# Performance work log

Measured on AMD Instinct MI355X. Metric: run time of the kernel, lower is better.

## Reference

```python
import jax, jax.numpy as jnp
import numpy as np

B, S, D, H = 2, 2048, 1024, 16

def setup_inputs() -> dict:
    key = jax.random.key(0)
    ks = jax.random.split(key, 5)
    s = 0.02
    return {
        "x": jax.random.normal(ks[0], (B, S, D), dtype=jnp.float32),
        "Wq": jax.random.normal(ks[1], (D, D), dtype=jnp.float32) * s,
        "bq": jnp.zeros((D,), dtype=jnp.float32),
        "Wk": jax.random.normal(ks[2], (D, D), dtype=jnp.float32) * s,
        "bk": jnp.zeros((D,), dtype=jnp.float32),
        "Wv": jax.random.normal(ks[3], (D, D), dtype=jnp.float32) * s,
        "bv": jnp.zeros((D,), dtype=jnp.float32),
        "Wp": jax.random.normal(ks[4], (D, D), dtype=jnp.float32) * s,
        "bp": jnp.zeros((D,), dtype=jnp.float32),
    }

def reference(x, Wq, bq, Wk, bk, Wv, bv, Wp, bp):
    b, s, d = x.shape
    hd = d // H
    # QKV projections, split into heads: [b, H, s, hd]
    q = (x @ Wq.T + bq).reshape(b, s, H, hd).transpose(0, 2, 1, 3)
    k = (x @ Wk.T + bk).reshape(b, s, H, hd).transpose(0, 2, 1, 3)
    v = (x @ Wv.T + bv).reshape(b, s, H, hd).transpose(0, 2, 1, 3)
    # NOTE: original scales by 1/sqrt(embedding_size), not head_dim
    att = jnp.einsum("bhqd,bhkd->bhqk", q, k) / jnp.sqrt(jnp.float32(d))
    causal = jnp.tril(jnp.ones((s, s), dtype=bool))
    att = jnp.where(causal[None, None], att, -jnp.inf)
    att = jax.nn.softmax(att, axis=-1)
    y = jnp.einsum("bhqk,bhkd->bhqd", att, v)
    y = y.transpose(0, 2, 1, 3).reshape(b, s, d)
    return y @ Wp.T + bp
```

## Files before the change

### kernel.cpp

```cpp
#include <hip/hip_runtime.h>
#include <hip/hip_bf16.h>

#define B_  2
#define S_  2048
#define D_  1024
#define H_  16
#define HD_ 64

typedef float  f32x4 __attribute__((ext_vector_type(4)));
typedef __bf16 bf16x8 __attribute__((ext_vector_type(8)));

__device__ __forceinline__ unsigned short f2bf(float f) {
    __bf16 h = (__bf16)f;
    return __builtin_bit_cast(unsigned short, h);
}

__device__ __forceinline__ void gload_lds16(const unsigned short* g, unsigned short* l) {
    __builtin_amdgcn_global_load_lds(
        (const __attribute__((address_space(1))) unsigned int*)g,
        (__attribute__((address_space(3))) unsigned int*)l, 16, 0, 0);
}

__global__ __launch_bounds__(256) void cvt5(
    const float* __restrict__ x,  const float* __restrict__ wq,
    const float* __restrict__ wk, const float* __restrict__ wv,
    const float* __restrict__ wp,
    unsigned short* __restrict__ xb, unsigned short* __restrict__ wqkv,
    unsigned short* __restrict__ wpb)
{
    const int bid = blockIdx.x;
    const float* src; unsigned short* dst; int off;
    if (bid < 4096)      { src = x;  dst = xb;              off = bid * 1024; }
    else if (bid < 5120) { src = wq; dst = wqkv;            off = (bid - 4096) * 1024; }
    else if (bid < 6144) { src = wk; dst = wqkv + (1<<20);  off = (bid - 5120) * 1024; }
    else if (bid < 7168) { src = wv; dst = wqkv + (2<<20);  off = (bid - 6144) * 1024; }
    else                 { src = wp; dst = wpb;             off = (bid - 7168) * 1024; }
    const int i = off + threadIdx.x * 4;
    float4 v = *reinterpret_cast<const float4*>(src + i);
    ushort4 o;
    o.x = f2bf(v.x); o.y = f2bf(v.y); o.z = f2bf(v.z); o.w = f2bf(v.w);
    *reinterpret_cast<ushort4*>(dst + i) = o;
}

__global__ __launch_bounds__(256, 3) void gemm128_qkv(
    const unsigned short* __restrict__ A,
    const unsigned short* __restrict__ Bm,
    const float* __restrict__ bias,
    void* __restrict__ C0, void* __restrict__ C1, void* __restrict__ C2,
    int M, int N, int K)
{
    __shared__ unsigned short As[128 * 64];
    __shared__ unsigned short Bs[128 * 64];
    const int tid  = threadIdx.x;
    const int lane = tid & 63;
    const int w    = tid >> 6;
    const int wm   = w >> 1, wn = w & 1;
    const int m0   = blockIdx.x << 7, n0 = blockIdx.y << 7;
    const int l15  = lane & 15, l4 = lane >> 4;
    const int r8   = lane >> 3;
    const int c8   = (lane & 7) << 3;

    f32x4 acc[4][4] = {};

    for (int k0 = 0; k0 < K; k0 += 64) {
        if (k0) __syncthreads();
        #pragma unroll
        for (int i = 0; i < 4; ++i) {
            const int row = i * 32 + w * 8;
            gload_lds16(A  + (size_t)(m0 + row + r8) * K + k0 + c8, As + row * 64);
            gload_lds16(Bm + (size_t)(n0 + row + r8) * K + k0 + c8, Bs + row * 64);
        }
        __syncthreads();
        #pragma unroll
        for (int kk = 0; kk < 2; ++kk) {
            bf16x8 af[4], bf[4];
            #pragma unroll
            for (int mi = 0; mi < 4; ++mi)
                af[mi] = *reinterpret_cast<const bf16x8*>(&As[(wm * 64 + mi * 16 + l15) * 64 + kk * 32 + l4 * 8]);
            #pragma unroll
            for (int ni = 0; ni < 4; ++ni)
                bf[ni] = *reinterpret_cast<const bf16x8*>(&Bs[(wn * 64 + ni * 16 + l15) * 64 + kk * 32 + l4 * 8]);
            #pragma unroll
            for (int mi = 0; mi < 4; ++mi)
                #pragma unroll
                for (int ni = 0; ni < 4; ++ni)
                    acc[mi][ni] = __builtin_amdgcn_mfma_f32_16x16x32_bf16(af[mi], bf[ni], acc[mi][ni], 0, 0, 0);
        }
    }

    const int region = n0 >> 10;
    #pragma unroll
    for (int mi = 0; mi < 4; ++mi) {
        #pragma unroll
        for (int ni = 0; ni < 4; ++ni) {
            const int colg = n0 + wn * 64 + ni * 16 + l15;
            const float bv = bias[colg];
            const int rowb = m0 + wm * 64 + mi * 16 + l4 * 4;
            const int cl = colg & 1023;
            if (region < 2) {
                unsigned short* C = (unsigned short*)(region ? C1 : C0);
                #pragma unroll
                for (int j = 0; j < 4; ++j)
                    C[(size_t)(rowb + j) * 1024 + cl] = f2bf(acc[mi][ni][j] + bv);
            } else {
                ushort4 pk;
                pk.x = f2bf(acc[mi][ni][0] + bv);
                pk.y = f2bf(acc[mi][ni][1] + bv);
                pk.z = f2bf(acc[mi][ni][2] + bv);
                pk.w = f2bf(acc[mi][ni][3] + bv);
                const int bb = rowb >> 11, s = rowb & (S_ - 1);
                unsigned short* vt = (unsigned short*)C2 +
                    ((size_t)(bb * H_ + (cl >> 6)) * HD_ + (cl & 63)) * S_ + s;
                *reinterpret_cast<ushort4*>(vt) = pk;
            }
        }
    }
}

__global__ __launch_bounds__(256, 2) void gemm64_proj(
    const unsigned short* __restrict__ A,
    const unsigned short* __restrict__ Bm,
    const float* __restrict__ bias,
    float* __restrict__ C,
    int M, int N, int K)
{
    __shared__ unsigned short As[64 * 64];
    __shared__ unsigned short Bs[128 * 64];
    const int tid  = threadIdx.x;
    const int lane = tid & 63;
    const int w    = tid >> 6;
    const int m0   = blockIdx.x << 6, n0 = blockIdx.y << 7;
    const int l15  = lane & 15, l4 = lane >> 4;
    const int r8   = lane >> 3;
    const int c8   = (lane & 7) << 3;

    f32x4 acc[4][2] = {};

    for (int k0 = 0; k0 < K; k0 += 64) {
        if (k0) __syncthreads();
        #pragma unroll
        for (int i = 0; i < 6; ++i) {
            const int c = w * 6 + i;
            if (c < 8)
                gload_lds16(A  + (size_t)(m0 + c * 8 + r8) * K + k0 + c8, As + c * 512);
            else
                gload_lds16(Bm + (size_t)(n0 + (c - 8) * 8 + r8) * K + k0 + c8, Bs + (c - 8) * 512);
        }
        __syncthreads();
        #pragma unroll
        for (int kk = 0; kk < 2; ++kk) {
            bf16x8 af[4], bf[2];
            #pragma unroll
            for (int mi = 0; mi < 4; ++mi)
                af[mi] = *reinterpret_cast<const bf16x8*>(&As[(mi * 16 + l15) * 64 + kk * 32 + l4 * 8]);
            #pragma unroll
            for (int ni = 0; ni < 2; ++ni)
                bf[ni] = *reinterpret_cast<const bf16x8*>(&Bs[(w * 32 + ni * 16 + l15) * 64 + kk * 32 + l4 * 8]);
            #pragma unroll
            for (int mi = 0; mi < 4; ++mi)
                #pragma unroll
                for (int ni = 0; ni < 2; ++ni)
                    acc[mi][ni] = __builtin_amdgcn_mfma_f32_16x16x32_bf16(af[mi], bf[ni], acc[mi][ni], 0, 0, 0);
        }
    }

    #pragma unroll
    for (int mi = 0; mi < 4; ++mi) {
        #pragma unroll
        for (int ni = 0; ni < 2; ++ni) {
            const int colg = n0 + w * 32 + ni * 16 + l15;
            const float bv = bias[colg];
            const int rowb = m0 + mi * 16 + l4 * 4;
            #pragma unroll
            for (int j = 0; j < 4; ++j)
                C[(size_t)(rowb + j) * N + colg] = acc[mi][ni][j] + bv;
        }
    }
}

#define SC_ 0.04508422f
__global__ __launch_bounds__(64, 2) void attn7(
    const unsigned short* __restrict__ qb,
    const unsigned short* __restrict__ kb,
    const unsigned short* __restrict__ vt,
    unsigned short* __restrict__ yb)
{
    __shared__ unsigned short Plds[32][88];

    const int lane = threadIdx.x;
    const int l15  = lane & 15, l4 = lane >> 4;

    const int bid  = blockIdx.x;
    const int xcd  = bid & 7;
    const int idx  = bid >> 3;
    const int hb   = xcd * 4 + (idx >> 6);
    const int j32  = idx & 31;
    const int qi   = ((idx >> 5) & 1) ? j32 : 63 - j32;
    const int h    = hb & 15, b = hb >> 4;

    const int q0w  = qi * 32;
    const size_t baseTok = (size_t)b * S_;
    const unsigned short* kgh = kb + baseTok * D_ + h * HD_;
    const unsigned short* vth = vt + (size_t)(b * H_ + h) * HD_ * S_;

    bf16x8 qf[2][2];
    #pragma unroll
    for (int m = 0; m < 2; ++m)
        #pragma unroll
        for (int kh = 0; kh < 2; ++kh)
            qf[m][kh] = *reinterpret_cast<const bf16x8*>(
                qb + (baseTok + q0w + m * 16 + l15) * D_ + h * HD_ + kh * 32 + l4 * 8);

    f32x4 o_acc[2][4] = {};
    float l_part[2][4] = {};

    const int nkv = (q0w + 95) >> 6;

    bf16x8 kf[4][2];
    #pragma unroll
    for (int kvb = 0; kvb < 4; ++kvb)
        #pragma unroll
        for (int kh = 0; kh < 2; ++kh)
            kf[kvb][kh] = *reinterpret_cast<const bf16x8*>(
                kgh + (size_t)(kvb * 16 + l15) * D_ + kh * 32 + l4 * 8);

    for (int t = 0; t < nkv; ++t) {
        const int kv0 = t << 6;
        const bool last = (t == nkv - 1);

        f32x4 s0[4] = {}, s1[4] = {};
        __builtin_amdgcn_s_setprio(1);
        #pragma unroll
        for (int kvb = 0; kvb < 4; ++kvb)
            #pragma unroll
            for (int kh = 0; kh < 2; ++kh)
                s0[kvb] = __builtin_amdgcn_mfma_f32_16x16x32_bf16(
                    qf[0][kh], kf[kvb][kh], s0[kvb], 0, 0, 0);
        #pragma unroll
        for (int kvb = 0; kvb < 4; ++kvb)
            #pragma unroll
            for (int kh = 0; kh < 2; ++kh)
                s1[kvb] = __builtin_amdgcn_mfma_f32_16x16x32_bf16(
                    qf[1][kh], kf[kvb][kh], s1[kvb], 0, 0, 0);
        __builtin_amdgcn_s_setprio(0);

        if (t + 1 < nkv) {
            #pragma unroll
            for (int kvb = 0; kvb < 4; ++kvb)
                #pragma unroll
                for (int kh = 0; kh < 2; ++kh)
                    kf[kvb][kh] = *reinterpret_cast<const bf16x8*>(
                        kgh + (size_t)(kv0 + 64 + kvb * 16 + l15) * D_ + kh * 32 + l4 * 8);
        }

        bf16x8 vf0[4];
        #pragma unroll
        for (int nb = 0; nb < 4; ++nb)
            vf0[nb] = *reinterpret_cast<const bf16x8*>(
                vth + (size_t)(nb * 16 + l15) * S_ + kv0 + l4 * 8);

        const int r = l4 * 4;
        if (!last) {
            #pragma unroll
            for (int j = 0; j < 4; ++j) {
                float p0 = exp2f(s0[0][j] * SC_), p1 = exp2f(s0[1][j] * SC_);
                float p2 = exp2f(s0[2][j] * SC_), p3 = exp2f(s0[3][j] * SC_);
                l_part[0][j] += (p0 + p1) + (p2 + p3);
                Plds[r + j][l15]      = f2bf(p0);
                Plds[r + j][16 + l15] = f2bf(p1);
                Plds[r + j][32 + l15] = f2bf(p2);
                Plds[r + j][48 + l15] = f2bf(p3);
            }
            #pragma unroll
            for (int j = 0; j < 4; ++j) {
                float p0 = exp2f(s1[0][j] * SC_), p1 = exp2f(s1[1][j] * SC_);
                float p2 = exp2f(s1[2][j] * SC_), p3 = exp2f(s1[3][j] * SC_);
                l_part[1][j] += (p0 + p1) + (p2 + p3);
                Plds[16 + r + j][l15]      = f2bf(p0);
                Plds[16 + r + j][16 + l15] = f2bf(p1);
                Plds[16 + r + j][32 + l15] = f2bf(p2);
                Plds[16 + r + j][48 + l15] = f2bf(p3);
            }
        } else {
            #pragma unroll
            for (int j = 0; j < 4; ++j) {
                const int rowg = q0w + r + j;
                float p[4];
                #pragma unroll
                for (int kvb = 0; kvb < 4; ++kvb) {
                    const bool ok = (kv0 + kvb * 16 + l15 <= rowg);
                    p[kvb] = ok ? exp2f(s0[kvb][j] * SC_) : 0.f;
                    Plds[r + j][kvb * 16 + l15] = f2bf(p[kvb]);
                }
                l_part[0][j] += (p[0] + p[1]) + (p[2] + p[3]);
            }
            #pragma unroll
            for (int j = 0; j < 4; ++j) {
                const int rowg = q0w + 16 + r + j;
                float p[4];
                #pragma unroll
                for (int kvb = 0; kvb < 4; ++kvb) {
                    const bool ok = (kv0 + kvb * 16 + l15 <= rowg);
                    p[kvb] = ok ? exp2f(s1[kvb][j] * SC_) : 0.f;
                    Plds[16 + r + j][kvb * 16 + l15] = f2bf(p[kvb]);
                }
                l_part[1][j] += (p[0] + p[1]) + (p[2] + p[3]);
            }
        }

        bf16x8 vf1[4];
        #pragma unroll
        for (int nb = 0; nb < 4; ++nb)
            vf1[nb] = *reinterpret_cast<const bf16x8*>(
                vth + (size_t)(nb * 16 + l15) * S_ + kv0 + 32 + l4 * 8);

        {
            bf16x8 pf0 = *reinterpret_cast<const bf16x8*>(&Plds[l15][l4 * 8]);
            bf16x8 pf1 = *reinterpret_cast<const bf16x8*>(&Plds[16 + l15][l4 * 8]);
            __builtin_amdgcn_s_setprio(1);
            #pragma unroll
            for (int nb = 0; nb < 4; ++nb) {
                o_acc[0][nb] = __builtin_amdgcn_mfma_f32_16x16x32_bf16(pf0, vf0[nb], o_acc[0][nb], 0, 0, 0);
                o_acc[1][nb] = __builtin_amdgcn_mfma_f32_16x16x32_bf16(pf1, vf0[nb], o_acc[1][nb], 0, 0, 0);
            }
            __builtin_amdgcn_s_setprio(0);
        }
        {
            bf16x8 pf0 = *reinterpret_cast<const bf16x8*>(&Plds[l15][32 + l4 * 8]);
            bf16x8 pf1 = *reinterpret_cast<const bf16x8*>(&Plds[16 + l15][32 + l4 * 8]);
            __builtin_amdgcn_s_setprio(1);
            #pragma unroll
            for (int nb = 0; nb < 4; ++nb) {
                o_acc[0][nb] = __builtin_amdgcn_mfma_f32_16x16x32_bf16(pf0, vf1[nb], o_acc[0][nb], 0, 0, 0);
                o_acc[1][nb] = __builtin_amdgcn_mfma_f32_16x16x32_bf16(pf1, vf1[nb], o_acc[1][nb], 0, 0, 0);
            }
            __builtin_amdgcn_s_setprio(0);
        }
    }

    float l[8];
    #pragma unroll
    for (int m = 0; m < 2; ++m)
        #pragma unroll
        for (int j = 0; j < 4; ++j)
            l[m * 4 + j] = l_part[m][j];
    #pragma unroll
    for (int st = 1; st <= 8; st <<= 1) {
        float tv[8];
        #pragma unroll
        for (int i = 0; i < 8; ++i) tv[i] = __shfl_xor(l[i], st);
        #pragma unroll
        for (int i = 0; i < 8; ++i) l[i] += tv[i];
    }
    #pragma unroll
    for (int m = 0; m < 2; ++m) {
        #pragma unroll
        for (int j = 0; j < 4; ++j) {
            const float inv = 1.0f / l[m * 4 + j];
            const int rowg = q0w + m * 16 + l4 * 4 + j;
            unsigned short* yp = yb + (baseTok + rowg) * D_ + h * HD_ + l15;
            #pragma unroll
            for (int nb = 0; nb < 4; ++nb)
                yp[nb * 16] = f2bf(o_acc[m][nb][j] * inv);
        }
    }
}

extern "C" void kernel_launch(void* const* d_in, const int* in_sizes, int n_in,
                              void* d_out, int out_size, void* d_ws, size_t ws_size,
                              hipStream_t stream)
{
    const float* x  = (const float*)d_in[0];
    const float* Wq = (const float*)d_in[1];
    const float* bq = (const float*)d_in[2];
    const float* Wk = (const float*)d_in[3];
    const float* bk = (const float*)d_in[4];
    const float* Wv = (const float*)d_in[5];
    const float* bv = (const float*)d_in[6];
    const float* Wp = (const float*)d_in[7];
    const float* bp = (const float*)d_in[8];

    char* ws = (char*)d_ws;
    const size_t MB = 1024 * 1024;
    unsigned short* xb    = (unsigned short*)(ws);
    unsigned short* wqkvb = (unsigned short*)(ws + 8 * MB);
    unsigned short* wpb   = (unsigned short*)(ws + 14 * MB);
    unsigned short* qbuf  = (unsigned short*)(ws + 16 * MB);
    unsigned short* kbuf  = (unsigned short*)(ws + 24 * MB);
    unsigned short* vtbf  = (unsigned short*)(ws + 32 * MB);
    unsigned short* ybuf  = (unsigned short*)(ws + 40 * MB);
    float*          bcat  = (float*)(ws + 48 * MB);

    const int M = B_ * S_;

    cvt5<<<8192, 256, 0, stream>>>(x, Wq, Wk, Wv, Wp, xb, wqkvb, wpb);
    hipMemcpyAsync(bcat,          bq, D_ * sizeof(float), hipMemcpyDeviceToDevice, stream);
    hipMemcpyAsync(bcat + D_,     bk, D_ * sizeof(float), hipMemcpyDeviceToDevice, stream);
    hipMemcpyAsync(bcat + 2 * D_, bv, D_ * sizeof(float), hipMemcpyDeviceToDevice, stream);

    gemm128_qkv<<<dim3(M / 128, 3072 / 128, 1), 256, 0, stream>>>(
        xb, wqkvb, bcat, qbuf, kbuf, vtbf, M, 3072, D_);

    attn7<<<2048, 64, 0, stream>>>(qbuf, kbuf, vtbf, ybuf);

    gemm64_proj<<<dim3(M / 64, D_ / 128, 1), 256, 0, stream>>>(
        ybuf, wpb, bp, (float*)d_out, M, D_, D_);
}
```

Baseline: 219.3 us.

## Split attention KV range across two blocks and add combine kernel

The attention kernel now splits each query tile's causal KV range into two halves handled by separate blocks. Each block writes unnormalized partial outputs (bf16) and row sums to workspace, and a new combine kernel adds them and normalizes. The goal is more parallelism and better balance for the long causal rows, with occupancy hint raised to 4. The bias copies are also folded into the conversion kernel to remove three memcpy launches. In exchange it adds an extra launch, extra global traffic, and rounding of the partial outputs to bf16 before they are summed.

```diff
diff --git a/kernel.cpp b/kernel.cpp
--- a/kernel.cpp
+++ b/kernel.cpp
@@ -14,6 +14,9 @@
     __bf16 h = (__bf16)f;
     return __builtin_bit_cast(unsigned short, h);
 }
+__device__ __forceinline__ float bf2f(unsigned short u) {
+    return (float)__builtin_bit_cast(__bf16, u);
+}
 
 __device__ __forceinline__ void gload_lds16(const unsigned short* g, unsigned short* l) {
     __builtin_amdgcn_global_load_lds(
@@ -24,11 +27,19 @@
 __global__ __launch_bounds__(256) void cvt5(
     const float* __restrict__ x,  const float* __restrict__ wq,
     const float* __restrict__ wk, const float* __restrict__ wv,
-    const float* __restrict__ wp,
+    const float* __restrict__ wp, const float* __restrict__ bq,
+    const float* __restrict__ bk, const float* __restrict__ bv,
     unsigned short* __restrict__ xb, unsigned short* __restrict__ wqkv,
-    unsigned short* __restrict__ wpb)
+    unsigned short* __restrict__ wpb, float* __restrict__ bcat)
 {
     const int bid = blockIdx.x;
+    if (bid >= 8192) {
+        const float* s = (bid == 8192) ? bq : (bid == 8193) ? bk : bv;
+        const int i = threadIdx.x * 4;
+        *reinterpret_cast<float4*>(bcat + (bid - 8192) * 1024 + i) =
+            *reinterpret_cast<const float4*>(s + i);
+        return;
+    }
     const float* src; unsigned short* dst; int off;
     if (bid < 4096)      { src = x;  dst = xb;              off = bid * 1024; }
     else if (bid < 5120) { src = wq; dst = wqkv;            off = (bid - 4096) * 1024; }
@@ -179,11 +190,12 @@
 }
 
 #define SC_ 0.04508422f
-__global__ __launch_bounds__(64, 2) void attn7(
+__global__ __launch_bounds__(64, 4) void attn8(
     const unsigned short* __restrict__ qb,
     const unsigned short* __restrict__ kb,
     const unsigned short* __restrict__ vt,
-    unsigned short* __restrict__ yb)
+    unsigned short* __restrict__ opart,
+    float* __restrict__ lpart)
 {
     __shared__ unsigned short Plds[32][88];
 
@@ -193,9 +205,12 @@
     const int bid  = blockIdx.x;
     const int xcd  = bid & 7;
     const int idx  = bid >> 3;
-    const int hb   = xcd * 4 + (idx >> 6);
-    const int j32  = idx & 31;
-    const int qi   = ((idx >> 5) & 1) ? j32 : 63 - j32;
+    const int hb   = xcd * 4 + (idx >> 7);
+    const int rem  = idx & 127;
+    const int sp   = rem >> 6;
+    const int j    = rem & 63;
+    const int j32  = j & 31;
+    const int qi   = ((j >> 5) & 1) ? j32 : 63 - j32;
     const int h    = hb & 15, b = hb >> 4;
 
     const int q0w  = qi * 32;
@@ -203,6 +218,11 @@
     const unsigned short* kgh = kb + baseTok * D_ + h * HD_;
     const unsigned short* vth = vt + (size_t)(b * H_ + h) * HD_ * S_;
 
+    const int nkv  = (q0w + 95) >> 6;
+    const int half = (nkv + 1) >> 1;
+    const int t0   = sp ? half : 0;
+    const int t1   = sp ? nkv  : half;
+
     bf16x8 qf[2][2];
     #pragma unroll
     for (int m = 0; m < 2; ++m)
@@ -214,136 +234,137 @@
     f32x4 o_acc[2][4] = {};
     float l_part[2][4] = {};
 
-    const int nkv = (q0w + 95) >> 6;
-
-    bf16x8 kf[4][2];
-    #pragma unroll
-    for (int kvb = 0; kvb < 4; ++kvb)
-        #pragma unroll
-        for (int kh = 0; kh < 2; ++kh)
-            kf[kvb][kh] = *reinterpret_cast<const bf16x8*>(
-                kgh + (size_t)(kvb * 16 + l15) * D_ + kh * 32 + l4 * 8);
-
-    for (int t = 0; t < nkv; ++t) {
-        const int kv0 = t << 6;
-        const bool last = (t == nkv - 1);
-
-        f32x4 s0[4] = {}, s1[4] = {};
-        __builtin_amdgcn_s_setprio(1);
+    if (t0 < t1) {
+        bf16x8 kf[4][2];
         #pragma unroll
         for (int kvb = 0; kvb < 4; ++kvb)
             #pragma unroll
             for (int kh = 0; kh < 2; ++kh)
-                s0[kvb] = __builtin_amdgcn_mfma_f32_16x16x32_bf16(
-                    qf[0][kh], kf[kvb][kh], s0[kvb], 0, 0, 0);
-        #pragma unroll
-        for (int kvb = 0; kvb < 4; ++kvb)
-            #pragma unroll
-            for (int kh = 0; kh < 2; ++kh)
-                s1[kvb] = __builtin_amdgcn_mfma_f32_16x16x32_bf16(
-                    qf[1][kh], kf[kvb][kh], s1[kvb], 0, 0, 0);
-        __builtin_amdgcn_s_setprio(0);
-
-        if (t + 1 < nkv) {
+                kf[kvb][kh] = *reinterpret_cast<const bf16x8*>(
+                    kgh + (size_t)(t0 * 64 + kvb * 16 + l15) * D_ + kh * 32 + l4 * 8);
+
+        for (int t = t0; t < t1; ++t) {
+            const int kv0 = t << 6;
+            const bool last = (t == nkv - 1);
+
+            f32x4 s0[4] = {}, s1[4] = {};
+            __builtin_amdgcn_s_setprio(1);
             #pragma unroll
             for (int kvb = 0; kvb < 4; ++kvb)
                 #pragma unroll
                 for (int kh = 0; kh < 2; ++kh)
-                    kf[kvb][kh] = *reinterpret_cast<const bf16x8*>(
-                        kgh + (size_t)(kv0 + 64 + kvb * 16 + l15) * D_ + kh * 32 + l4 * 8);
-        }
-
-        bf16x8 vf0[4];
-        #pragma unroll
-        for (int nb = 0; nb < 4; ++nb)
-            vf0[nb] = *reinterpret_cast<const bf16x8*>(
-                vth + (size_t)(nb * 16 + l15) * S_ + kv0 + l4 * 8);
-
-        const int r = l4 * 4;
-        if (!last) {
-            #pragma unroll
-            for (int j = 0; j < 4; ++j) {
-                float p0 = exp2f(s0[0][j] * SC_), p1 = exp2f(s0[1][j] * SC_);
-                float p2 = exp2f(s0[2][j] * SC_), p3 = exp2f(s0[3][j] * SC_);
-                l_part[0][j] += (p0 + p1) + (p2 + p3);
-                Plds[r + j][l15]      = f2bf(p0);
-                Plds[r + j][16 + l15] = f2bf(p1);
-                Plds[r + j][32 + l15] = f2bf(p2);
-                Plds[r + j][48 + l15] = f2bf(p3);
+                    s0[kvb] = __builtin_amdgcn_mfma_f32_16x16x32_bf16(
+                        qf[0][kh], kf[kvb][kh], s0[kvb], 0, 0, 0);
+            #pragma unroll
+            for (int kvb = 0; kvb < 4; ++kvb)
+                #pragma unroll
+                for (int kh = 0; kh < 2; ++kh)
+                    s1[kvb] = __builtin_amdgcn_mfma_f32_16x16x32_bf16(
+                        qf[1][kh], kf[kvb][kh], s1[kvb], 0, 0, 0);
+            __builtin_amdgcn_s_setprio(0);
+
+            if (t + 1 < t1) {
+                #pragma unroll
+                for (int kvb = 0; kvb < 4; ++kvb)
+                    #pragma unroll
+                    for (int kh = 0; kh < 2; ++kh)
+                        kf[kvb][kh] = *reinterpret_cast<const bf16x8*>(
+                            kgh + (size_t)(kv0 + 64 + kvb * 16 + l15) * D_ + kh * 32 + l4 * 8);
             }
-            #pragma unroll
-            for (int j = 0; j < 4; ++j) {
-                float p0 = exp2f(s1[0][j] * SC_), p1 = exp2f(s1[1][j] * SC_);
-                float p2 = exp2f(s1[2][j] * SC_), p3 = exp2f(s1[3][j] * SC_);
-                l_part[1][j] += (p0 + p1) + (p2 + p3);
-                Plds[16 + r + j][l15]      = f2bf(p0);
-                Plds[16 + r + j][16 + l15] = f2bf(p1);
-                Plds[16 + r + j][32 + l15] = f2bf(p2);
-                Plds[16 + r + j][48 + l15] = f2bf(p3);
+
+            bf16x8 vf0[4];
+            #pragma unroll
+            for (int nb = 0; nb < 4; ++nb)
+                vf0[nb] = *reinterpret_cast<const bf16x8*>(
+                    vth + (size_t)(nb * 16 + l15) * S_ + kv0 + l4 * 8);
+
+            const int r = l4 * 4;
+            if (!last) {
+                #pragma unroll
+                for (int jj = 0; jj < 4; ++jj) {
+                    float p0 = exp2f(s0[0][jj] * SC_), p1 = exp2f(s0[1][jj] * SC_);
+                    float p2 = exp2f(s0[2][jj] * SC_), p3 = exp2f(s0[3][jj] * SC_);
+                    l_part[0][jj] += (p0 + p1) + (p2 + p3);
+                    Plds[r + jj][l15]      = f2bf(p0);
+                    Plds[r + jj][16 + l15] = f2bf(p1);
+                    Plds[r + jj][32 + l15] = f2bf(p2);
+                    Plds[r + jj][48 + l15] = f2bf(p3);
+                }
+                #pragma unroll
+                for (int jj = 0; jj < 4; ++jj) {
+                    float p0 = exp2f(s1[0][jj] * SC_), p1 = exp2f(s1[1][jj] * SC_);
+                    float p2 = exp2f(s1[2][jj] * SC_), p3 = exp2f(s1[3][jj] * SC_);
+                    l_part[1][jj] += (p0 + p1) + (p2 + p3);
+                    Plds[16 + r + jj][l15]      = f2bf(p0);
+                    Plds[16 + r + jj][16 + l15] = f2bf(p1);
+                    Plds[16 + r + jj][32 + l15] = f2bf(p2);
+                    Plds[16 + r + jj][48 + l15] = f2bf(p3);
+                }
+            } else {
+                #pragma unroll
+                for (int jj = 0; jj < 4; ++jj) {
+                    const int rowg = q0w + r + jj;
+                    float p[4];
+                    #pragma unroll
+                    for (int kvb = 0; kvb < 4; ++kvb) {
+                        const bool ok = (kv0 + kvb * 16 + l15 <= rowg);
+                        p[kvb] = ok ? exp2f(s0[kvb][jj] * SC_) : 0.f;
+                        Plds[r + jj][kvb * 16 + l15] = f2bf(p[kvb]);
+                    }
+                    l_part[0][jj] += (p[0] + p[1]) + (p[2] + p[3]);
+                }
+                #pragma unroll
+                for (int jj = 0; jj < 4; ++jj) {
+                    const int rowg = q0w + 16 + r + jj;
+                    float p[4];
+                    #pragma unroll
+                    for (int kvb = 0; kvb < 4; ++kvb) {
+                        const bool ok = (kv0 + kvb * 16 + l15 <= rowg);
+                        p[kvb] = ok ? exp2f(s1[kvb][jj] * SC_) : 0.f;
+                        Plds[16 + r + jj][kvb * 16 + l15] = f2bf(p[kvb]);
+                    }
+                    l_part[1][jj] += (p[0] + p[1]) + (p[2] + p[3]);
+                }
             }
-        } else {
-            #pragma unroll
-            for (int j = 0; j < 4; ++j) {
-                const int rowg = q0w + r + j;
-                float p[4];
-                #pragma unroll
-                for (int kvb = 0; kvb < 4; ++kvb) {
-                    const bool ok = (kv0 + kvb * 16 + l15 <= rowg);
-                    p[kvb] = ok ? exp2f(s0[kvb][j] * SC_) : 0.f;
-                    Plds[r + j][kvb * 16 + l15] = f2bf(p[kvb]);
-                }
-                l_part[0][j] += (p[0] + p[1]) + (p[2] + p[3]);
+
+            bf16x8 vf1[4];
+            #pragma unroll
+            for (int nb = 0; nb < 4; ++nb)
+                vf1[nb] = *reinterpret_cast<const bf16x8*>(
+                    vth + (size_t)(nb * 16 + l15) * S_ + kv0 + 32 + l4 * 8);
+
+            {
+                bf16x8 pf0 = *reinterpret_cast<const bf16x8*>(&Plds[l15][l4 * 8]);
+                bf16x8 pf1 = *reinterpret_cast<const bf16x8*>(&Plds[16 + l15][l4 * 8]);
+                __builtin_amdgcn_s_setprio(1);
+                #pragma unroll
+                for (int nb = 0; nb < 4; ++nb) {
+                    o_acc[0][nb] = __builtin_amdgcn_mfma_f32_16x16x32_bf16(pf0, vf0[nb], o_acc[0][nb], 0, 0, 0);
+                    o_acc[1][nb] = __builtin_amdgcn_mfma_f32_16x16x32_bf16(pf1, vf0[nb], o_acc[1][nb], 0, 0, 0);
+                }
+                __builtin_amdgcn_s_setprio(0);
             }
-            #pragma unroll
-            for (int j = 0; j < 4; ++j) {
-                const int rowg = q0w + 16 + r + j;
-                float p[4];
-                #pragma unroll
-                for (int kvb = 0; kvb < 4; ++kvb) {
-                    const bool ok = (kv0 + kvb * 16 + l15 <= rowg);
-                    p[kvb] = ok ? exp2f(s1[kvb][j] * SC_) : 0.f;
-                    Plds[16 + r + j][kvb * 16 + l15] = f2bf(p[kvb]);
-                }
-                l_part[1][j] += (p[0] + p[1]) + (p[2] + p[3]);
+            {
+                bf16x8 pf0 = *reinterpret_cast<const bf16x8*>(&Plds[l15][32 + l4 * 8]);
+                bf16x8 pf1 = *reinterpret_cast<const bf16x8*>(&Plds[16 + l15][32 + l4 * 8]);
+                __builtin_amdgcn_s_setprio(1);
+                #pragma unroll
+                for (int nb = 0; nb < 4; ++nb) {
+                    o_acc[0][nb] = __builtin_amdgcn_mfma_f32_16x16x32_bf16(pf0, vf1[nb], o_acc[0][nb], 0, 0, 0);
+                    o_acc[1][nb] = __builtin_amdgcn_mfma_f32_16x16x32_bf16(pf1, vf1[nb], o_acc[1][nb], 0, 0, 0);
+                }
+                __builtin_amdgcn_s_setprio(0);
             }
         }
-
-        bf16x8 vf1[4];
-        #pragma unroll
-        for (int nb = 0; nb < 4; ++nb)
-            vf1[nb] = *reinterpret_cast<const bf16x8*>(
-                vth + (size_t)(nb * 16 + l15) * S_ + kv0 + 32 + l4 * 8);
-
-        {
-            bf16x8 pf0 = *reinterpret_cast<const bf16x8*>(&Plds[l15][l4 * 8]);
-            bf16x8 pf1 = *reinterpret_cast<const bf16x8*>(&Plds[16 + l15][l4 * 8]);
-            __builtin_amdgcn_s_setprio(1);
-            #pragma unroll
-            for (int nb = 0; nb < 4; ++nb) {
-                o_acc[0][nb] = __builtin_amdgcn_mfma_f32_16x16x32_bf16(pf0, vf0[nb], o_acc[0][nb], 0, 0, 0);
-                o_acc[1][nb] = __builtin_amdgcn_mfma_f32_16x16x32_bf16(pf1, vf0[nb], o_acc[1][nb], 0, 0, 0);
-            }
-            __builtin_amdgcn_s_setprio(0);
-        }
-        {
-            bf16x8 pf0 = *reinterpret_cast<const bf16x8*>(&Plds[l15][32 + l4 * 8]);
-            bf16x8 pf1 = *reinterpret_cast<const bf16x8*>(&Plds[16 + l15][32 + l4 * 8]);
-            __builtin_amdgcn_s_setprio(1);
-            #pragma unroll
-            for (int nb = 0; nb < 4; ++nb) {
-                o_acc[0][nb] = __builtin_amdgcn_mfma_f32_16x16x32_bf16(pf0, vf1[nb], o_acc[0][nb], 0, 0, 0);
-                o_acc[1][nb] = __builtin_amdgcn_mfma_f32_16x16x32_bf16(pf1, vf1[nb], o_acc[1][nb], 0, 0, 0);
-            }
-            __builtin_amdgcn_s_setprio(0);
-        }
-    }
-
+    }
+
+    const int slot = (hb * 64 + qi) * 2 + sp;
     float l[8];
     #pragma unroll
     for (int m = 0; m < 2; ++m)
         #pragma unroll
-        for (int j = 0; j < 4; ++j)
-            l[m * 4 + j] = l_part[m][j];
+        for (int jj = 0; jj < 4; ++jj)
+            l[m * 4 + jj] = l_part[m][jj];
     #pragma unroll
     for (int st = 1; st <= 8; st <<= 1) {
         float tv[8];
@@ -352,17 +373,42 @@
         #pragma unroll
         for (int i = 0; i < 8; ++i) l[i] += tv[i];
     }
-    #pragma unroll
-    for (int m = 0; m < 2; ++m) {
-        #pragma unroll
-        for (int j = 0; j < 4; ++j) {
-            const float inv = 1.0f / l[m * 4 + j];
-            const int rowg = q0w + m * 16 + l4 * 4 + j;
-            unsigned short* yp = yb + (baseTok + rowg) * D_ + h * HD_ + l15;
-            #pragma unroll
-            for (int nb = 0; nb < 4; ++nb)
-                yp[nb * 16] = f2bf(o_acc[m][nb][j] * inv);
-        }
+    if (l15 == 0) {
+        float* lp = lpart + slot * 32;
+        #pragma unroll
+        for (int m = 0; m < 2; ++m)
+            #pragma unroll
+            for (int jj = 0; jj < 4; ++jj)
+                lp[m * 16 + l4 * 4 + jj] = l[m * 4 + jj];
+    }
+    unsigned short* op = opart + (size_t)slot * 2048;
+    #pragma unroll
+    for (int m = 0; m < 2; ++m)
+        #pragma unroll
+        for (int nb = 0; nb < 4; ++nb)
+            #pragma unroll
+            for (int jj = 0; jj < 4; ++jj)
+                op[(m * 16 + l4 * 4 + jj) * 64 + nb * 16 + l15] = f2bf(o_acc[m][nb][jj]);
+}
+
+__global__ __launch_bounds__(64) void attn_combine(
+    const unsigned short* __restrict__ opart,
+    const float* __restrict__ lpart,
+    unsigned short* __restrict__ yb)
+{
+    const int g   = blockIdx.x;
+    const int hb  = g >> 6, qi = g & 63;
+    const int b   = hb >> 4, h = hb & 15;
+    const int lane = threadIdx.x;
+    const unsigned short* op0 = opart + (size_t)(g * 2) * 2048;
+    const unsigned short* op1 = op0 + 2048;
+    const float* lp0 = lpart + g * 2 * 32;
+    const float* lp1 = lp0 + 32;
+    #pragma unroll 4
+    for (int row = 0; row < 32; ++row) {
+        const float o = bf2f(op0[row * 64 + lane]) + bf2f(op1[row * 64 + lane]);
+        const float l = lp0[row] + lp1[row];
+        yb[((size_t)(b * S_ + qi * 32 + row)) * D_ + h * HD_ + lane] = f2bf(o / l);
     }
 }
 
@@ -384,24 +430,24 @@
     const size_t MB = 1024 * 1024;
     unsigned short* xb    = (unsigned short*)(ws);
     unsigned short* wqkvb = (unsigned short*)(ws + 8 * MB);
-    unsigned short* wpb   = (unsigned short*)(ws + 14 * MB);
+    unsigned short* opart = (unsigned short*)(ws);
     unsigned short* qbuf  = (unsigned short*)(ws + 16 * MB);
     unsigned short* kbuf  = (unsigned short*)(ws + 24 * MB);
     unsigned short* vtbf  = (unsigned short*)(ws + 32 * MB);
     unsigned short* ybuf  = (unsigned short*)(ws + 40 * MB);
-    float*          bcat  = (float*)(ws + 48 * MB);
+    unsigned short* wpb   = (unsigned short*)(ws + 48 * MB);
+    float*          bcat  = (float*)(ws + 50 * MB);
+    float*          lpart = (float*)(ws + 50 * MB + 65536);
 
     const int M = B_ * S_;
 
-    cvt5<<<8192, 256, 0, stream>>>(x, Wq, Wk, Wv, Wp, xb, wqkvb, wpb);
-    hipMemcpyAsync(bcat,          bq, D_ * sizeof(float), hipMemcpyDeviceToDevice, stream);
-    hipMemcpyAsync(bcat + D_,     bk, D_ * sizeof(float), hipMemcpyDeviceToDevice, stream);
-    hipMemcpyAsync(bcat + 2 * D_, bv, D_ * sizeof(float), hipMemcpyDeviceToDevice, stream);
+    cvt5<<<8195, 256, 0, stream>>>(x, Wq, Wk, Wv, Wp, bq, bk, bv, xb, wqkvb, wpb, bcat);
 
     gemm128_qkv<<<dim3(M / 128, 3072 / 128, 1), 256, 0, stream>>>(
         xb, wqkvb, bcat, qbuf, kbuf, vtbf, M, 3072, D_);
 
-    attn7<<<2048, 64, 0, stream>>>(qbuf, kbuf, vtbf, ybuf);
+    attn8<<<4096, 64, 0, stream>>>(qbuf, kbuf, vtbf, opart, lpart);
+    attn_combine<<<2048, 64, 0, stream>>>(opart, lpart, ybuf);
 
     gemm64_proj<<<dim3(M / 64, D_ / 128, 1), 256, 0, stream>>>(
         ybuf, wpb, bp, (float*)d_out, M, D_, D_);
```

Measured after the change: 335.3 us. +52.9%, slower.
